# Kernel tuning notes

Hardware: AMD Instinct MI355X
Metric: run time of the kernel (lower is better)

Reference implementation:

```python
import jax, jax.numpy as jnp
import numpy as np

HEAD_DIM = 128
NUM_HEADS = 16
CONTEXT_LENGTH = 4096
THETA_BASE = 10000.0


def precompute_rope(head_dim, context_length, theta_base=THETA_BASE):
    inv_freq = 1.0 / theta_base ** (jnp.arange(0, head_dim, 2, dtype=jnp.float32) / head_dim)
    positions = jnp.arange(context_length, dtype=jnp.float32)
    angles = positions[:, None] * inv_freq[None, :]          # [T, hd/2]
    angles = jnp.concatenate([angles, angles], axis=1)       # [T, hd]
    return jnp.cos(angles), jnp.sin(angles)


def apply_rope(x, cos, sin):
    # x: [b, h, s, hd]
    s, hd = x.shape[2], x.shape[3]
    x1, x2 = x[..., : hd // 2], x[..., hd // 2 :]
    rotated = jnp.concatenate([-x2, x1], axis=-1)
    return (x * cos[None, None, :s, :] + rotated * sin[None, None, :s, :]).astype(x.dtype)


def setup_inputs() -> dict:
    key = jax.random.key(0)
    ks = jax.random.split(key, 5)
    b, s, d = 2, 2048, 2048
    scale = 1.0 / np.sqrt(d)
    return {
        "x": jax.random.normal(ks[0], (b, s, d), dtype=jnp.float32),
        "Wq": jax.random.normal(ks[1], (d, d), dtype=jnp.float32) * scale,
        "Wk": jax.random.normal(ks[2], (d, d), dtype=jnp.float32) * scale,
        "Wv": jax.random.normal(ks[3], (d, d), dtype=jnp.float32) * scale,
        "Wo": jax.random.normal(ks[4], (d, d), dtype=jnp.float32) * scale,
    }


def reference(x, Wq, Wk, Wv, Wo):
    b, s, d = x.shape
    h, hd = NUM_HEADS, HEAD_DIM
    cos, sin = precompute_rope(hd, CONTEXT_LENGTH)

    q = (x @ Wq).reshape(b, s, h, hd).transpose(0, 2, 1, 3)  # [b,h,s,hd]
    k = (x @ Wk).reshape(b, s, h, hd).transpose(0, 2, 1, 3)
    v = (x @ Wv).reshape(b, s, h, hd).transpose(0, 2, 1, 3)

    q = apply_rope(q, cos, sin)
    k = apply_rope(k, cos, sin)

    scores = jnp.einsum("bhqd,bhkd->bhqk", q, k)             # [b,h,s,s]
    causal = jnp.tril(jnp.ones((s, s), dtype=bool))
    scores = jnp.where(causal[None, None], scores, -jnp.inf)
    weights = jax.nn.softmax(scores / np.sqrt(hd), axis=-1)
    ctx = jnp.einsum("bhqk,bhkd->bhqd", weights, v)          # [b,h,s,hd]
    ctx = ctx.transpose(0, 2, 1, 3).reshape(b, s, d)
    return ctx @ Wo
```

## Files before the change

### kernel.cpp

```cpp
#include <hip/hip_runtime.h>
#include <hip/hip_bf16.h>

typedef __attribute__((ext_vector_type(8))) __bf16 bf16x8;
typedef __attribute__((ext_vector_type(8))) short  short8;
typedef __attribute__((ext_vector_type(4))) float  f32x4;
typedef unsigned short u16;
typedef unsigned int   u32;

__device__ __forceinline__ u16 f2bf(float f) {
  u32 u = __builtin_bit_cast(u32, f);
  u += 0x7fffu + ((u >> 16) & 1u);
  return (u16)(u >> 16);
}
__device__ __forceinline__ float bf2f(u16 h) {
  return __builtin_bit_cast(float, (u32)h << 16);
}

#define MFMA_BF16(a, b, c) __builtin_amdgcn_mfma_f32_16x16x32_bf16( \
    __builtin_bit_cast(bf16x8, (a)), __builtin_bit_cast(bf16x8, (b)), (c), 0, 0, 0)

__device__ __forceinline__ void gload_lds16(const void* g, void* l) {
  __builtin_amdgcn_global_load_lds(
      (const __attribute__((address_space(1))) void*)g,
      (__attribute__((address_space(3))) void*)l, 16, 0, 0);
}

#define SEQ   2048
#define DMODEL 2048
#define NH    16
#define HD    128

static constexpr size_t SZ_MAT   = 4096ull * 2048 * 2;
static constexpr size_t OFF_XB   = 0;
static constexpr size_t OFF_WQKVT= OFF_XB   + SZ_MAT;
static constexpr size_t OFF_WOT  = OFF_WQKVT+ 3ull*2048*2048*2;
static constexpr size_t OFF_Q    = OFF_WOT  + 2048ull*2048*2;
static constexpr size_t OFF_K    = OFF_Q    + SZ_MAT;
static constexpr size_t OFF_VT   = OFF_K    + SZ_MAT;
static constexpr size_t OFF_CTX  = OFF_VT   + SZ_MAT;
static constexpr size_t OFF_COS  = OFF_CTX  + SZ_MAT;
static constexpr size_t OFF_SIN  = OFF_COS  + 2048ull*64*4;
static constexpr size_t WS_NEED  = OFF_SIN  + 2048ull*64*4;

__global__ void cast_x_kernel(const float* __restrict__ x, u16* __restrict__ xb, int n4) {
  int id = blockIdx.x * blockDim.x + threadIdx.x;
  if (id >= n4) return;
  float4 v = ((const float4*)x)[id];
  ushort4 o;
  o.x = f2bf(v.x); o.y = f2bf(v.y); o.z = f2bf(v.z); o.w = f2bf(v.w);
  ((ushort4*)xb)[id] = o;
}

__global__ void castT_w_kernel(const float* __restrict__ W0, const float* __restrict__ W1,
                               const float* __restrict__ W2, const float* __restrict__ W3,
                               u16* __restrict__ Wqkvt, u16* __restrict__ Wot) {
  __shared__ float tile[32][33];
  int z = blockIdx.z;
  const float* W = (z == 0) ? W0 : (z == 1) ? W1 : (z == 2) ? W2 : W3;
  u16* Out = (z < 3) ? (Wqkvt + (size_t)z * 2048 * 2048) : Wot;
  int n0 = blockIdx.x * 32, k0 = blockIdx.y * 32;
  int tx = threadIdx.x, ty = threadIdx.y;
  #pragma unroll
  for (int i = 0; i < 4; i++)
    tile[ty + 8 * i][tx] = W[(size_t)(k0 + ty + 8 * i) * 2048 + n0 + tx];
  __syncthreads();
  #pragma unroll
  for (int i = 0; i < 4; i++)
    Out[(size_t)(n0 + ty + 8 * i) * 2048 + k0 + tx] = f2bf(tile[tx][ty + 8 * i]);
}

__global__ void rope_table_kernel(float* __restrict__ ct, float* __restrict__ st) {
  int id = blockIdx.x * blockDim.x + threadIdx.x;
  int pos = id >> 6, j = id & 63;
  float inv = exp2f(-(float)j * (13.287712379549449f / 64.0f));
  float a = (float)pos * inv;
  ct[id] = cosf(a);
  st[id] = sinf(a);
}

__global__ void rope_apply_kernel(u16* __restrict__ Q, u16* __restrict__ K,
                                  const float* __restrict__ ct, const float* __restrict__ st) {
  int id = blockIdx.x * blockDim.x + threadIdx.x;
  u16* P = blockIdx.y ? K : Q;
  int row = id >> 10;
  int r = id & 1023;
  int hh = r >> 6, j = r & 63;
  int pos = row & 2047;
  size_t base = (size_t)row * 2048 + hh * 128 + j;
  float x1 = bf2f(P[base]), x2 = bf2f(P[base + 64]);
  float c = ct[pos * 64 + j], s = st[pos * 64 + j];
  P[base]      = f2bf(x1 * c - x2 * s);
  P[base + 64] = f2bf(x2 * c + x1 * s);
}

#define SB __builtin_amdgcn_sched_barrier(0)
#define BAR()   do { SB; __builtin_amdgcn_s_barrier(); SB; } while (0)
#define VMCNT4() do { SB; asm volatile("s_waitcnt vmcnt(4)" ::: "memory"); SB; } while (0)
#define VMCNT0() do { SB; asm volatile("s_waitcnt vmcnt(0)" ::: "memory"); SB; } while (0)

#define STAGE8(gb, kt, H, lb)                                                  \
  do { _Pragma("unroll")                                                       \
    for (int u = 0; u < 2; u++) {                                              \
      int c = tid + u * 512;                                                   \
      int rr = c >> 3, sl = c & 7;                                             \
      gload_lds16((gb) + (size_t)((H) * 128 + rr) * 4096 + (size_t)(kt) * 128  \
                       + ((sl ^ (rr & 7)) << 4),                               \
                  (lb) + (H) * 16384 + c * 16);                                \
    } } while (0)

#define LDA8(lb, MG)                                                           \
  do { _Pragma("unroll")                                                       \
    for (int mi = 0; mi < 4; mi++) {                                           \
      af[mi][0] = *(const short8*)((lb) + aoff + ((MG) + mi) * 2048 + sw0);    \
      af[mi][1] = *(const short8*)((lb) + aoff + ((MG) + mi) * 2048 + sw1);    \
    } } while (0)

#define LDB4(lb, NG)                                                           \
  do { _Pragma("unroll")                                                       \
    for (int nj = 0; nj < 2; nj++) {                                           \
      bfr[(NG) + nj][0] = *(const short8*)((lb) + boff + ((NG) + nj) * 2048 + sw0); \
      bfr[(NG) + nj][1] = *(const short8*)((lb) + boff + ((NG) + nj) * 2048 + sw1); \
    } } while (0)

#define MMQ(MG, NG)                                                            \
  do {                                                                         \
    __builtin_amdgcn_s_setprio(1);                                             \
    _Pragma("unroll")                                                          \
    for (int mi = 0; mi < 4; mi++) {                                           \
      _Pragma("unroll")                                                        \
      for (int nj = 0; nj < 2; nj++) {                                         \
        acc[(MG) + mi][(NG) + nj] =                                            \
            MFMA_BF16(af[mi][0], bfr[(NG) + nj][0], acc[(MG) + mi][(NG) + nj]);\
        acc[(MG) + mi][(NG) + nj] =                                            \
            MFMA_BF16(af[mi][1], bfr[(NG) + nj][1], acc[(MG) + mi][(NG) + nj]);\
      }                                                                        \
    }                                                                          \
    __builtin_amdgcn_s_setprio(0);                                             \
  } while (0)

#define GEMM8_ITER(K1v, K2v, K3v, LAST)                                        \
  do {                                                                         \
    LDA8(A0p, 0); LDB4(B0p, 0);                                                \
    STAGE8(Ab, (K1v), 0, A1p);                                                 \
    BAR(); MMQ(0, 0); BAR();                                                   \
    LDB4(B0p, 2);                                                              \
    STAGE8(Ab, (K1v), 1, A1p);                                                 \
    BAR(); MMQ(0, 2); BAR();                                                   \
    LDA8(A0p, 4);                                                              \
    if (!(LAST)) STAGE8(Bb, (K2v), 0, B0p);                                    \
    BAR(); MMQ(4, 2); BAR();                                                   \
    if (!(LAST)) STAGE8(Ab, (K2v), 0, A0p);                                    \
    if (LAST) { VMCNT0(); } else { VMCNT4(); }                                 \
    BAR(); MMQ(4, 0); BAR();                                                   \
    LDA8(A1p, 0); LDB4(B1p, 0);                                                \
    if (!(LAST)) STAGE8(Ab, (K2v), 1, A0p);                                    \
    BAR(); MMQ(0, 0); BAR();                                                   \
    LDB4(B1p, 2);                                                              \
    if (!(LAST)) STAGE8(Bb, (K2v), 1, B0p);                                    \
    BAR(); MMQ(0, 2); BAR();                                                   \
    LDA8(A1p, 4);                                                              \
    if (!(LAST)) STAGE8(Bb, (K3v), 0, B1p);                                    \
    BAR(); MMQ(4, 2); BAR();                                                   \
    if (!(LAST)) { STAGE8(Bb, (K3v), 1, B1p); VMCNT4(); }                      \
    BAR(); MMQ(4, 0); BAR();                                                   \
  } while (0)

__global__ __launch_bounds__(512, 2)
void gemm8_qkv_kernel(const u16* __restrict__ A, const u16* __restrict__ Bt,
                      u16* __restrict__ Qo, u16* __restrict__ Ko,
                      u16* __restrict__ Vto) {
  __shared__ u16 Asm[2][16384];
  __shared__ u16 Bsm[2][16384];
  const int tid = threadIdx.x;
  const int lane = tid & 63, w = tid >> 6;
  const int grp = lane >> 4, lr = lane & 15;
  const int wm = w >> 2, wn = w & 3;
  const int bm = blockIdx.y, bn = blockIdx.x;

  const char* Ab = (const char*)A + (size_t)bm * 256 * 4096;
  const char* Bb = (const char*)Bt + (size_t)bn * 256 * 4096;
  char* A0p = (char*)Asm[0]; char* A1p = (char*)Asm[1];
  char* B0p = (char*)Bsm[0]; char* B1p = (char*)Bsm[1];

  f32x4 acc[8][4] = {};
  short8 af[4][2], bfr[4][2];
  const int aoff = wm * 16384 + lr * 128;
  const int boff = wn * 8192 + lr * 128;
  const int sw0 = ((grp    ) ^ (lr & 7)) << 4;
  const int sw1 = ((grp + 4) ^ (lr & 7)) << 4;

  STAGE8(Ab, 0, 0, A0p);
  STAGE8(Ab, 0, 1, A0p);
  STAGE8(Bb, 0, 0, B0p);
  STAGE8(Bb, 0, 1, B0p);
  STAGE8(Bb, 1, 0, B1p);
  STAGE8(Bb, 1, 1, B1p);
  VMCNT4();
  BAR();

  #pragma unroll 1
  for (int t = 0; t < 15; ++t) {
    GEMM8_ITER(2 * t + 1, 2 * t + 2, 2 * t + 3, false);
  }
  GEMM8_ITER(31, 0, 0, true);

  const int seg = bn >> 3;
  const int row0 = bm * 256 + wm * 128 + grp * 4;
  const int col0 = (bn & 7) * 256 + wn * 64 + lr;
  if (seg < 2) {
    u16* O = seg ? Ko : Qo;
    #pragma unroll
    for (int ai = 0; ai < 8; ai++)
      #pragma unroll
      for (int nj = 0; nj < 4; nj++) {
        int col = col0 + nj * 16;
        int row = row0 + ai * 16;
        #pragma unroll
        for (int r = 0; r < 4; r++)
          O[(size_t)(row + r) * 2048 + col] = f2bf(acc[ai][nj][r]);
      }
  } else {
    #pragma unroll
    for (int ai = 0; ai < 8; ai++) {
      int row = row0 + ai * 16;
      int b = row >> 11, s = row & 2047;
      int sp = (s & ~31) | (((s >> 2) & 3) << 3) | (((s >> 4) & 1) << 2);
      #pragma unroll
      for (int nj = 0; nj < 4; nj++) {
        int colv = col0 + nj * 16;
        ushort4 o;
        o.x = f2bf(acc[ai][nj][0]); o.y = f2bf(acc[ai][nj][1]);
        o.z = f2bf(acc[ai][nj][2]); o.w = f2bf(acc[ai][nj][3]);
        *(ushort4*)(Vto + (size_t)(b * 2048 + colv) * 2048 + sp) = o;
      }
    }
  }
}

__global__ __launch_bounds__(256)
void gemm_bt_kernel(const u16* __restrict__ A, const u16* __restrict__ Bt,
                    float* __restrict__ Co, int K) {
  __shared__ u16 Al[128 * 32];
  __shared__ u16 Bl[128 * 32];
  const int tid = threadIdx.x;
  const int lane = tid & 63;
  const int w = tid >> 6;
  const int grp = lane >> 4, lr = lane & 15;
  const int bm = blockIdx.y, bn = blockIdx.x;
  const int wm = w >> 1, wn = w & 1;
  f32x4 acc[4][4] = {};
  const char* Ab = (const char*)(A + (size_t)bm * 128 * K);
  const char* Bb = (const char*)(Bt + (size_t)bn * 128 * K);
  const int c0 = tid, c1 = tid + 256;
  const int rA0 = c0 >> 2, cb0 = (c0 & 3) * 16;
  const int rA1 = c1 >> 2, cb1 = (c1 & 3) * 16;

  for (int kt = 0; kt < K; kt += 32) {
    gload_lds16(Ab + (size_t)rA0 * K * 2 + kt * 2 + cb0, (char*)Al + c0 * 16);
    gload_lds16(Ab + (size_t)rA1 * K * 2 + kt * 2 + cb1, (char*)Al + c1 * 16);
    gload_lds16(Bb + (size_t)rA0 * K * 2 + kt * 2 + cb0, (char*)Bl + c0 * 16);
    gload_lds16(Bb + (size_t)rA1 * K * 2 + kt * 2 + cb1, (char*)Bl + c1 * 16);
    __syncthreads();
    short8 af[4], bf[4];
    #pragma unroll
    for (int mi = 0; mi < 4; mi++)
      af[mi] = *(const short8*)(Al + (wm * 64 + mi * 16 + lr) * 32 + grp * 8);
    #pragma unroll
    for (int nj = 0; nj < 4; nj++)
      bf[nj] = *(const short8*)(Bl + (wn * 64 + nj * 16 + lr) * 32 + grp * 8);
    #pragma unroll
    for (int mi = 0; mi < 4; mi++)
      #pragma unroll
      for (int nj = 0; nj < 4; nj++)
        acc[mi][nj] = MFMA_BF16(af[mi], bf[nj], acc[mi][nj]);
    __syncthreads();
  }

  const int rowBase = bm * 128 + wm * 64 + grp * 4;
  const int colBase = bn * 128 + wn * 64 + lr;
  #pragma unroll
  for (int mi = 0; mi < 4; mi++)
    #pragma unroll
    for (int nj = 0; nj < 4; nj++)
      #pragma unroll
      for (int r = 0; r < 4; r++)
        Co[(size_t)(rowBase + mi * 16 + r) * 2048 + colBase + nj * 16] = acc[mi][nj][r];
}

__global__ __launch_bounds__(512, 4)
void attn_kernel(const u16* __restrict__ Q, const u16* __restrict__ K,
                 const u16* __restrict__ Vt, u16* __restrict__ ctx) {
  __shared__ u16 Kl[2][64 * 128];
  __shared__ u16 Vl[2][128 * 64];
  const int qt = blockIdx.x, bh = blockIdx.y;
  const int b = bh >> 4, h = bh & 15;
  const int tid = threadIdx.x;
  const int w = tid >> 6, lane = tid & 63;
  const int grp = lane >> 4, lr = lane & 15;
  const int q0w = qt * 128 + w * 16;
  const int qrow = q0w + lr;
  const u16* Qp = Q + ((size_t)(b * 2048 + qrow)) * 2048 + h * 128;
  short8 qf[4];
  #pragma unroll
  for (int kk = 0; kk < 4; kk++)
    qf[kk] = *(const short8*)(Qp + kk * 32 + grp * 8);

  f32x4 acc_o[8] = {};
  float m_run = -3.0e38f, l_run = 0.0f;
  const float ce = 0.08838834764831845f * 1.4426950408889634f;

  const char* Kbh = (const char*)K  + ((size_t)b * 2048 * 2048 + h * 128) * 2;
  const char* Vbh = (const char*)Vt + ((size_t)(b * 2048 + h * 128)) * 2048 * 2;

  auto stage = [&](int buf, int kvt) {
    const int kv0 = kvt * 64;
    #pragma unroll
    for (int u = 0; u < 2; u++) {
      int c = tid + u * 512;
      int row = c >> 4, slot = c & 15;
      gload_lds16(Kbh + (size_t)(kv0 + row) * 4096 + ((slot ^ (row & 7)) << 4),
                  (char*)Kl[buf] + c * 16);
    }
    #pragma unroll
    for (int u = 0; u < 2; u++) {
      int c = tid + u * 512;
      int dd = c >> 3, slot = c & 7;
      gload_lds16(Vbh + (size_t)dd * 4096 + kv0 * 2 + ((slot ^ (dd & 7)) << 4),
                  (char*)Vl[buf] + c * 16);
    }
  };

  const int nkv = 2 * qt + 2;
  stage(0, 0);
  __syncthreads();

  for (int kvt = 0; kvt < nkv; kvt++) {
    const int kv0 = kvt * 64;
    const int cur = kvt & 1;
    if (kvt + 1 < nkv) stage(cur ^ 1, kvt + 1);

    if (kv0 <= q0w + 15) {
      const char* Kc = (const char*)Kl[cur];
      const char* Vc = (const char*)Vl[cur];
      f32x4 sa[4] = {};
      #pragma unroll
      for (int kk = 0; kk < 4; kk++) {
        #pragma unroll
        for (int mi = 0; mi < 4; mi++) {
          const int krow = mi * 16 + lr;
          short8 kf = *(const short8*)(Kc + krow * 256 + (((kk * 4 + grp) ^ (krow & 7)) << 4));
          sa[mi] = MFMA_BF16(kf, qf[kk], sa[mi]);
        }
      }
      float tmax = -3.0e38f;
      const bool dg = (kv0 + 63 > qrow);
      #pragma unroll
      for (int mi = 0; mi < 4; mi++)
        #pragma unroll
        for (int r = 0; r < 4; r++) {
          float s = sa[mi][r];
          if (dg && (kv0 + mi * 16 + grp * 4 + r > qrow)) s = -3.0e38f;
          sa[mi][r] = s;
          tmax = fmaxf(tmax, s);
        }
      tmax = fmaxf(tmax, __shfl_xor(tmax, 16, 64));
      tmax = fmaxf(tmax, __shfl_xor(tmax, 32, 64));
      const float m_new = fmaxf(m_run, tmax);
      const float alpha = exp2f((m_run - m_new) * ce);
      float psum = 0.0f;
      #pragma unroll
      for (int mi = 0; mi < 4; mi++)
        #pragma unroll
        for (int r = 0; r < 4; r++) {
          float e = exp2f((sa[mi][r] - m_new) * ce);
          sa[mi][r] = e;
          psum += e;
        }
      psum += __shfl_xor(psum, 16, 64);
      psum += __shfl_xor(psum, 32, 64);
      l_run = l_run * alpha + psum;
      m_run = m_new;
      #pragma unroll
      for (int mi = 0; mi < 8; mi++) acc_o[mi] *= alpha;

      short8 pb[2];
      #pragma unroll
      for (int kb = 0; kb < 2; kb++)
        #pragma unroll
        for (int i = 0; i < 4; i++) {
          pb[kb][i]     = (short)f2bf(sa[2 * kb][i]);
          pb[kb][4 + i] = (short)f2bf(sa[2 * kb + 1][i]);
        }
      #pragma unroll
      for (int mi = 0; mi < 8; mi++) {
        const int vrow = mi * 16 + lr;
        #pragma unroll
        for (int kb = 0; kb < 2; kb++) {
          short8 vf = *(const short8*)(Vc + vrow * 128 + (((kb * 4 + grp) ^ (vrow & 7)) << 4));
          acc_o[mi] = MFMA_BF16(vf, pb[kb], acc_o[mi]);
        }
      }
    }
    __syncthreads();
  }

  const float inv_l = 1.0f / l_run;
  u16* Cp = ctx + ((size_t)(b * 2048 + qrow)) * 2048 + h * 128;
  #pragma unroll
  for (int mi = 0; mi < 8; mi++) {
    ushort4 o;
    o.x = f2bf(acc_o[mi][0] * inv_l);
    o.y = f2bf(acc_o[mi][1] * inv_l);
    o.z = f2bf(acc_o[mi][2] * inv_l);
    o.w = f2bf(acc_o[mi][3] * inv_l);
    *(ushort4*)(Cp + mi * 16 + grp * 4) = o;
  }
}

extern "C" void kernel_launch(void* const* d_in, const int* in_sizes, int n_in,
                              void* d_out, int out_size, void* d_ws, size_t ws_size,
                              hipStream_t stream) {
  const float* x  = (const float*)d_in[0];
  const float* Wq = (const float*)d_in[1];
  const float* Wk = (const float*)d_in[2];
  const float* Wv = (const float*)d_in[3];
  const float* Wo = (const float*)d_in[4];
  float* out = (float*)d_out;
  char* ws = (char*)d_ws;
  if (ws_size < WS_NEED) return;

  u16* xb    = (u16*)(ws + OFF_XB);
  u16* Wqkvt = (u16*)(ws + OFF_WQKVT);
  u16* Wot   = (u16*)(ws + OFF_WOT);
  u16* Qb    = (u16*)(ws + OFF_Q);
  u16* Kb    = (u16*)(ws + OFF_K);
  u16* Vtb   = (u16*)(ws + OFF_VT);
  u16* ctxb  = (u16*)(ws + OFF_CTX);
  float* ctab = (float*)(ws + OFF_COS);
  float* stab = (float*)(ws + OFF_SIN);

  cast_x_kernel<<<8192, 256, 0, stream>>>(x, xb, 2097152);
  castT_w_kernel<<<dim3(64, 64, 4), dim3(32, 8), 0, stream>>>(Wq, Wk, Wv, Wo, Wqkvt, Wot);
  rope_table_kernel<<<512, 256, 0, stream>>>(ctab, stab);
  gemm8_qkv_kernel<<<dim3(24, 16), 512, 0, stream>>>(xb, Wqkvt, Qb, Kb, Vtb);
  rope_apply_kernel<<<dim3(16384, 2), 256, 0, stream>>>(Qb, Kb, ctab, stab);
  attn_kernel<<<dim3(16, 32), 512, 0, stream>>>(Qb, Kb, Vtb, ctxb);
  gemm_bt_kernel<<<dim3(16, 32), 256, 0, stream>>>(ctxb, Wot, out, 2048);
}
```

Measured before the change: 445.2 us.

## Pair causal query tiles per block for balanced attention and lazy softmax rescale

Each attention block now processes two query tiles (qt and 15-qt), so every block does the same amount of causal work and the loaded K/V tiles are shared by both. The online softmax skips rescaling the accumulators unless the running max grows past a threshold. The grid is halved, launch bounds are relaxed to 2 blocks per CU, and explicit vmcnt waits with raw barriers replace __syncthreads. In exchange it doubles accumulator register usage and lowers occupancy.

```diff
diff --git a/kernel.cpp b/kernel.cpp
--- a/kernel.cpp
+++ b/kernel.cpp
@@ -287,27 +287,35 @@
         Co[(size_t)(rowBase + mi * 16 + r) * 2048 + colBase + nj * 16] = acc[mi][nj][r];
 }
 
-__global__ __launch_bounds__(512, 4)
+__global__ __launch_bounds__(512, 2)
 void attn_kernel(const u16* __restrict__ Q, const u16* __restrict__ K,
                  const u16* __restrict__ Vt, u16* __restrict__ ctx) {
   __shared__ u16 Kl[2][64 * 128];
   __shared__ u16 Vl[2][128 * 64];
-  const int qt = blockIdx.x, bh = blockIdx.y;
+  const int qtA = blockIdx.x, qtB = 15 - qtA;
+  const int bh = blockIdx.y;
   const int b = bh >> 4, h = bh & 15;
   const int tid = threadIdx.x;
   const int w = tid >> 6, lane = tid & 63;
   const int grp = lane >> 4, lr = lane & 15;
-  const int q0w = qt * 128 + w * 16;
-  const int qrow = q0w + lr;
-  const u16* Qp = Q + ((size_t)(b * 2048 + qrow)) * 2048 + h * 128;
-  short8 qf[4];
-  #pragma unroll
-  for (int kk = 0; kk < 4; kk++)
-    qf[kk] = *(const short8*)(Qp + kk * 32 + grp * 8);
-
-  f32x4 acc_o[8] = {};
-  float m_run = -3.0e38f, l_run = 0.0f;
+  const int q0A = qtA * 128 + w * 16, qrowA = q0A + lr;
+  const int q0B = qtB * 128 + w * 16, qrowB = q0B + lr;
+
+  short8 qfA[4], qfB[4];
+  {
+    const u16* QpA = Q + ((size_t)(b * 2048 + qrowA)) * 2048 + h * 128;
+    const u16* QpB = Q + ((size_t)(b * 2048 + qrowB)) * 2048 + h * 128;
+    #pragma unroll
+    for (int kk = 0; kk < 4; kk++) {
+      qfA[kk] = *(const short8*)(QpA + kk * 32 + grp * 8);
+      qfB[kk] = *(const short8*)(QpB + kk * 32 + grp * 8);
+    }
+  }
+
+  f32x4 accA[8] = {}, accB[8] = {};
+  float mA = -3.0e38f, lA = 0.0f, mB = -3.0e38f, lB = 0.0f;
   const float ce = 0.08838834764831845f * 1.4426950408889634f;
+  const float THR = 8.0f / ce;
 
   const char* Kbh = (const char*)K  + ((size_t)b * 2048 * 2048 + h * 128) * 2;
   const char* Vbh = (const char*)Vt + ((size_t)(b * 2048 + h * 128)) * 2048 * 2;
@@ -330,90 +338,108 @@
     }
   };
 
-  const int nkv = 2 * qt + 2;
+  auto process = [&](const short8* qf, f32x4* acc, float& m_run, float& l_run,
+                     int qrow, const char* Kc, const char* Vc, int kv0) {
+    f32x4 sa[4] = {};
+    #pragma unroll
+    for (int kk = 0; kk < 4; kk++) {
+      #pragma unroll
+      for (int mi = 0; mi < 4; mi++) {
+        const int krow = mi * 16 + lr;
+        short8 kf = *(const short8*)(Kc + krow * 256 + (((kk * 4 + grp) ^ (krow & 7)) << 4));
+        sa[mi] = MFMA_BF16(kf, qf[kk], sa[mi]);
+      }
+    }
+    float tmax = -3.0e38f;
+    const bool dg = (kv0 + 63 > qrow);
+    #pragma unroll
+    for (int mi = 0; mi < 4; mi++)
+      #pragma unroll
+      for (int r = 0; r < 4; r++) {
+        float s = sa[mi][r];
+        if (dg && (kv0 + mi * 16 + grp * 4 + r > qrow)) s = -3.0e38f;
+        sa[mi][r] = s;
+        tmax = fmaxf(tmax, s);
+      }
+    tmax = fmaxf(tmax, __shfl_xor(tmax, 16, 64));
+    tmax = fmaxf(tmax, __shfl_xor(tmax, 32, 64));
+    if (!__all(tmax <= m_run + THR)) {
+      const float m_new = fmaxf(m_run, tmax);
+      const float alpha = exp2f((m_run - m_new) * ce);
+      #pragma unroll
+      for (int mi = 0; mi < 8; mi++) acc[mi] *= alpha;
+      l_run *= alpha;
+      m_run = m_new;
+    }
+    float psum = 0.0f;
+    #pragma unroll
+    for (int mi = 0; mi < 4; mi++)
+      #pragma unroll
+      for (int r = 0; r < 4; r++) {
+        float e = exp2f((sa[mi][r] - m_run) * ce);
+        sa[mi][r] = e;
+        psum += e;
+      }
+    psum += __shfl_xor(psum, 16, 64);
+    psum += __shfl_xor(psum, 32, 64);
+    l_run += psum;
+
+    short8 pb[2];
+    #pragma unroll
+    for (int kb = 0; kb < 2; kb++)
+      #pragma unroll
+      for (int i = 0; i < 4; i++) {
+        pb[kb][i]     = (short)f2bf(sa[2 * kb][i]);
+        pb[kb][4 + i] = (short)f2bf(sa[2 * kb + 1][i]);
+      }
+    #pragma unroll
+    for (int mi = 0; mi < 8; mi++) {
+      const int vrow = mi * 16 + lr;
+      #pragma unroll
+      for (int kb = 0; kb < 2; kb++) {
+        short8 vf = *(const short8*)(Vc + vrow * 128 + (((kb * 4 + grp) ^ (vrow & 7)) << 4));
+        acc[mi] = MFMA_BF16(vf, pb[kb], acc[mi]);
+      }
+    }
+  };
+
+  const int ntiles = 2 * qtB + 2;
   stage(0, 0);
-  __syncthreads();
-
-  for (int kvt = 0; kvt < nkv; kvt++) {
+
+  #pragma unroll 1
+  for (int kvt = 0; kvt < ntiles; kvt++) {
     const int kv0 = kvt * 64;
     const int cur = kvt & 1;
-    if (kvt + 1 < nkv) stage(cur ^ 1, kvt + 1);
-
-    if (kv0 <= q0w + 15) {
-      const char* Kc = (const char*)Kl[cur];
-      const char* Vc = (const char*)Vl[cur];
-      f32x4 sa[4] = {};
-      #pragma unroll
-      for (int kk = 0; kk < 4; kk++) {
-        #pragma unroll
-        for (int mi = 0; mi < 4; mi++) {
-          const int krow = mi * 16 + lr;
-          short8 kf = *(const short8*)(Kc + krow * 256 + (((kk * 4 + grp) ^ (krow & 7)) << 4));
-          sa[mi] = MFMA_BF16(kf, qf[kk], sa[mi]);
-        }
-      }
-      float tmax = -3.0e38f;
-      const bool dg = (kv0 + 63 > qrow);
-      #pragma unroll
-      for (int mi = 0; mi < 4; mi++)
-        #pragma unroll
-        for (int r = 0; r < 4; r++) {
-          float s = sa[mi][r];
-          if (dg && (kv0 + mi * 16 + grp * 4 + r > qrow)) s = -3.0e38f;
-          sa[mi][r] = s;
-          tmax = fmaxf(tmax, s);
-        }
-      tmax = fmaxf(tmax, __shfl_xor(tmax, 16, 64));
-      tmax = fmaxf(tmax, __shfl_xor(tmax, 32, 64));
-      const float m_new = fmaxf(m_run, tmax);
-      const float alpha = exp2f((m_run - m_new) * ce);
-      float psum = 0.0f;
-      #pragma unroll
-      for (int mi = 0; mi < 4; mi++)
-        #pragma unroll
-        for (int r = 0; r < 4; r++) {
-          float e = exp2f((sa[mi][r] - m_new) * ce);
-          sa[mi][r] = e;
-          psum += e;
-        }
-      psum += __shfl_xor(psum, 16, 64);
-      psum += __shfl_xor(psum, 32, 64);
-      l_run = l_run * alpha + psum;
-      m_run = m_new;
-      #pragma unroll
-      for (int mi = 0; mi < 8; mi++) acc_o[mi] *= alpha;
-
-      short8 pb[2];
-      #pragma unroll
-      for (int kb = 0; kb < 2; kb++)
-        #pragma unroll
-        for (int i = 0; i < 4; i++) {
-          pb[kb][i]     = (short)f2bf(sa[2 * kb][i]);
-          pb[kb][4 + i] = (short)f2bf(sa[2 * kb + 1][i]);
-        }
-      #pragma unroll
-      for (int mi = 0; mi < 8; mi++) {
-        const int vrow = mi * 16 + lr;
-        #pragma unroll
-        for (int kb = 0; kb < 2; kb++) {
-          short8 vf = *(const short8*)(Vc + vrow * 128 + (((kb * 4 + grp) ^ (vrow & 7)) << 4));
-          acc_o[mi] = MFMA_BF16(vf, pb[kb], acc_o[mi]);
-        }
-      }
-    }
-    __syncthreads();
-  }
-
-  const float inv_l = 1.0f / l_run;
-  u16* Cp = ctx + ((size_t)(b * 2048 + qrow)) * 2048 + h * 128;
+    if (kvt + 1 < ntiles) {
+      stage(cur ^ 1, kvt + 1);
+      SB; asm volatile("s_waitcnt vmcnt(4)" ::: "memory"); SB;
+    } else {
+      SB; asm volatile("s_waitcnt vmcnt(0)" ::: "memory"); SB;
+    }
+    __builtin_amdgcn_s_barrier(); SB;
+
+    const char* Kc = (const char*)Kl[cur];
+    const char* Vc = (const char*)Vl[cur];
+    if (kv0 <= q0B + 15)
+      process(qfB, accB, mB, lB, qrowB, Kc, Vc, kv0);
+    if (kv0 <= q0A + 15)
+      process(qfA, accA, mA, lA, qrowA, Kc, Vc, kv0);
+
+    SB; __builtin_amdgcn_s_barrier(); SB;
+  }
+
+  const float invA = 1.0f / lA, invB = 1.0f / lB;
+  u16* CpA = ctx + ((size_t)(b * 2048 + qrowA)) * 2048 + h * 128;
+  u16* CpB = ctx + ((size_t)(b * 2048 + qrowB)) * 2048 + h * 128;
   #pragma unroll
   for (int mi = 0; mi < 8; mi++) {
-    ushort4 o;
-    o.x = f2bf(acc_o[mi][0] * inv_l);
-    o.y = f2bf(acc_o[mi][1] * inv_l);
-    o.z = f2bf(acc_o[mi][2] * inv_l);
-    o.w = f2bf(acc_o[mi][3] * inv_l);
-    *(ushort4*)(Cp + mi * 16 + grp * 4) = o;
+    ushort4 oa, ob;
+    oa.x = f2bf(accA[mi][0] * invA); oa.y = f2bf(accA[mi][1] * invA);
+    oa.z = f2bf(accA[mi][2] * invA); oa.w = f2bf(accA[mi][3] * invA);
+    ob.x = f2bf(accB[mi][0] * invB); ob.y = f2bf(accB[mi][1] * invB);
+    ob.z = f2bf(accB[mi][2] * invB); ob.w = f2bf(accB[mi][3] * invB);
+    *(ushort4*)(CpA + mi * 16 + grp * 4) = oa;
+    *(ushort4*)(CpB + mi * 16 + grp * 4) = ob;
   }
 }
 
@@ -444,6 +470,6 @@
   rope_table_kernel<<<512, 256, 0, stream>>>(ctab, stab);
   gemm8_qkv_kernel<<<dim3(24, 16), 512, 0, stream>>>(xb, Wqkvt, Qb, Kb, Vtb);
   rope_apply_kernel<<<dim3(16384, 2), 256, 0, stream>>>(Qb, Kb, ctab, stab);
-  attn_kernel<<<dim3(16, 32), 512, 0, stream>>>(Qb, Kb, Vtb, ctxb);
+  attn_kernel<<<dim3(8, 32), 512, 0, stream>>>(Qb, Kb, Vtb, ctxb);
   gemm_bt_kernel<<<dim3(16, 32), 256, 0, stream>>>(ctxb, Wot, out, 2048);
 }
```

Result: faster. 420.3 us (-5.6%).
